# Kernel optimization log

Hardware: AMD Instinct MI355X
Metric: run time of the kernel (lower is better)

The kernel has to match this reference:

```python
import jax, jax.numpy as jnp
from jax import lax
import numpy as np

MAX_ATOMS = 50
MAX_DEGREE = 4
MAX_RINGS = 16
BATCH = 16384
EDGE_KEEP_PROB = 0.3  # fraction of neighbor slots that are real edges; rest are -1 (masked)


def setup_inputs() -> dict:
    key = jax.random.key(0)
    k1, k2 = jax.random.split(key)
    e = jax.random.randint(k1, (BATCH, MAX_ATOMS, MAX_DEGREE), 0, MAX_ATOMS, dtype=jnp.int32)
    keep = jax.random.uniform(k2, (BATCH, MAX_ATOMS, MAX_DEGREE)) < EDGE_KEEP_PROB
    edge = jnp.where(keep, e, jnp.int32(-1))
    return {"edge": edge}


def reference(edge):
    B, A, D = edge.shape
    N = A + 1  # node 0 is the masked-edge sentinel after +1 shift and zero-row pad
    bidx = jnp.arange(B)
    # masked_edges: shift indices by +1, pad a zero row at atom index 0 -> [B, N, D]
    me = jnp.pad(edge.astype(jnp.int32) + 1, ((0, 0), (1, 0), (0, 0)))

    # per-node state, shape [B, N]
    lnf = jnp.ones((B, N), jnp.int32).at[:, 0].set(0).at[:, 1].set(0)  # leaf_not_found
    nnv = jnp.ones((B, N), jnp.int32).at[:, 0].set(0)                  # node_not_visited
    Tree = jnp.zeros((B, N), jnp.int32)                                 # parent pointers
    num_rings = jnp.zeros((B,), jnp.int32)
    ring_idx = jnp.zeros((B, N, 2), jnp.int32)

    def visit(state, visiting):
        lnf, nnv, Tree, num_rings, ring_idx = state
        for d in range(D):  # small static degree loop (4)
            nxt = me[bidx, visiting, d]                 # [B]
            slnf = lnf[bidx, nxt]                       # specific_leaf_not_found
            slnv = nnv[bidx, nxt]                       # specific_leaf_not_visited
            cyc = (1 - slnf) * slnv * (nxt != 0).astype(jnp.int32)  # cycle_found
            ring_idx = ring_idx.at[bidx, num_rings, 0].add(visiting * cyc)
            ring_idx = ring_idx.at[bidx, num_rings, 1].add(nxt * cyc)
            num_rings = num_rings + cyc
            Tree = Tree.at[bidx, nxt].add(slnf * visiting)
            lnf = lnf.at[bidx, nxt].set(0)
        nnv = nnv.at[bidx, visiting].set(0)
        return (lnf, nnv, Tree, num_rings, ring_idx)

    # atom_idx == 1: visit node 1 (special-cased init above)
    state = visit((lnf, nnv, Tree, num_rings, ring_idx), jnp.ones((B,), jnp.int32))

    def atom_body(_, state):
        lnf, nnv = state[0], state[1]
        visiting = jnp.argmax(nnv * (1 - lnf), axis=-1).astype(jnp.int32)
        return visit(state, visiting)

    state = lax.fori_loop(2, A + 1, atom_body, state)
    lnf, nnv, Tree, num_rings, ring_idx = state

    max_num_rings = jnp.max(num_rings)
    rings = jnp.zeros((B, MAX_RINGS, A), jnp.int32)

    def ring_body(carry):
        i, rings = carry
        air = jnp.zeros((B,), jnp.int32)  # atom_in_ring_idx

        # branch 0: mark ancestor chain of ring endpoint 0
        start = ring_idx[:, i, 0]
        vb0 = jnp.zeros((B, N), jnp.int32).at[bidx, start].set(1)
        def mark0(_, c):
            vb0, start = c
            nxt = Tree[bidx, start]
            return (vb0.at[bidx, nxt].set(1), nxt)
        vb0, _ = lax.fori_loop(0, A, mark0, (vb0, start))

        # branch 1: walk ancestor chain of endpoint 1, emit atoms until chains meet
        start = ring_idx[:, i, 1]
        vb1 = jnp.zeros((B, N), jnp.int32).at[bidx, start].set(1)
        rings = rings.at[bidx, i, air].set(start)
        def b1(_, c):
            rings, vb1, start, air = c
            nxt = Tree[bidx, start]
            same = jnp.any(vb0 * vb1 == 1, axis=-1)
            nsv = (~same).astype(jnp.int32)
            air = air + nsv
            rings = rings.at[bidx, i, air].add(nxt * nsv)
            vb1 = vb1.at[bidx, nxt].set(1)
            return (rings, vb1, nxt, air)
        rings, vb1, _, air = lax.fori_loop(0, A, b1, (rings, vb1, start, air))

        # branch 2: walk endpoint-0 chain again, emit atoms until it meets branch 1
        start = ring_idx[:, i, 0]
        vb0b = jnp.zeros((B, N), jnp.int32).at[bidx, start].set(1)
        air = air + 1
        rings = rings.at[bidx, i, air].set(start)
        def b2(_, c):
            rings, vb0b, start, air = c
            nxt = Tree[bidx, start]
            vb0b = vb0b.at[bidx, nxt].set(1)
            same = jnp.any(vb0b * vb1 == 1, axis=-1)
            nsv = (~same).astype(jnp.int32)
            air = air + nsv
            rings = rings.at[bidx, i, air].add(nxt * nsv)
            return (rings, vb0b, nxt, air)
        rings, _, _, _ = lax.fori_loop(0, A, b2, (rings, vb0b, start, air))
        return (i + 1, rings)

    def ring_cond(carry):
        return carry[0] < max_num_rings

    _, rings = lax.while_loop(ring_cond, ring_body, (jnp.int32(0), rings))
    return (Tree, ring_idx, rings - 1)
```

## Files before the change

kernel.cpp:

```cpp
#include <hip/hip_runtime.h>
#include <stdint.h>

constexpr int BATCH = 16384;
constexpr int A     = 50;
constexpr int NN    = 51;
constexpr int MAXR  = 16;
constexpr int EPW   = 8;
constexpr int WPB   = 4;

__global__ __launch_bounds__(WPB * 64)
void fused_kernel(const int* __restrict__ edge, int* __restrict__ out)
{
    const int lane  = threadIdx.x & 63;
    const int wid   = threadIdx.x >> 6;
    const int gbase = (blockIdx.x * WPB + wid) * EPW;

    __shared__ uint32_t eds[WPB][EPW][NN];
    __shared__ uint8_t  tre[WPB][EPW][52];
    __shared__ uint8_t  rg [WPB][EPW][104];

    {
        const uint4 z = make_uint4(0, 0, 0, 0);
        uint4* t16 = (uint4*)&tre[wid][0][0];
        if (lane < 26) t16[lane] = z;
        uint4* r16 = (uint4*)&rg[wid][0][0];
        if (lane < 52) r16[lane] = z;
    }
    {
        const int4* e4 = (const int4*)edge + (size_t)gbase * A;
        #pragma unroll
        for (int k = 0; k < 7; ++k) {
            const int gi = k * 64 + lane;
            if (gi < EPW * A) {
                const int4 v = e4[gi];
                const int el = gi / A, n = gi - A * el;
                eds[wid][el][n] = (uint32_t)(v.x + 1) | ((uint32_t)(v.y + 1) << 8)
                                | ((uint32_t)(v.z + 1) << 16) | ((uint32_t)(v.w + 1) << 24);
            }
        }
    }

    const int  e  = lane >> 3;
    const int  d8 = lane & 7;
    const int  d  = d8 & 3;
    const bool hi = d8 >= 4;

    uint64_t L = (((uint64_t)1 << NN) - 1) & ~(uint64_t)3;
    uint64_t V = (((uint64_t)1 << NN) - 1) & ~(uint64_t)1;
    uint64_t M = 2;
    int visiting = 1, nr = 0;
    uint32_t w = eds[wid][e][0];

    #pragma unroll 1
    for (int it = 0; it < A; ++it) {
        const int n0 = w & 0xff, n1 = (w >> 8) & 0xff, n2 = (w >> 16) & 0xff, n3 = w >> 24;
        const uint64_t bu = ((uint64_t)1 << n0) | ((uint64_t)1 << n1)
                          | ((uint64_t)1 << n2) | ((uint64_t)1 << n3);
        const int myn = (w >> (8 * d)) & 0xff;
        const uint64_t bm = (uint64_t)1 << myn;
        const uint64_t visbit = (uint64_t)1 << visiting;
        const uint64_t Mn = (M | (V & bu)) & ~visbit;
        const bool dn = (Mn == 0);
        const uint64_t Msafe = dn ? (uint64_t)2 : Mn;
        const int nv = (int)__builtin_ctzll(Msafe);
        const uint32_t wn = eds[wid][e][nv - 1];
        const bool dup = ((d > 0) & (myn == n0)) | ((d > 1) & (myn == n1)) | ((d > 2) & (myn == n2));
        const bool fa  = ((L & bm) == 0) | dup;
        const bool cf  = fa & ((V & bm) != 0) & (myn != 0);
        const bool cb  = cf & !hi;
        const uint64_t Bc = __ballot(cb);
        const uint32_t qb = (uint32_t)(Bc >> (lane & 56)) & 0xfu;
        const int slot = nr + __builtin_popcount(qb & ((1u << d) - 1));
        nr += __builtin_popcount(qb);
        tre[wid][e][(fa | hi) ? 51 : myn] = (uint8_t)visiting;
        *(uint16_t*)&rg[wid][e][(cf & hi & (slot < NN)) ? 2 * slot : 102] =
            (uint16_t)(visiting | (myn << 8));
        L &= ~bu;
        V &= ~visbit;
        M = Mn; visiting = nv;
        w = dn ? 0u : wn;
        if (__ballot(!dn) == 0) break;
    }

    int*  otree = out;
    int2* oridx = (int2*)(out + (size_t)BATCH * NN);

    #pragma unroll 1
    for (int e2 = 0; e2 < EPW; ++e2) {
        const int b = gbase + e2;
        const uint32_t pv = (lane < NN) ? *(const uint16_t*)&rg[wid][e2][2 * lane] : 0;
        const int f = (lane < NN) ? (int)tre[wid][e2][lane] : 0;
        if (lane < NN) {
            otree[(size_t)b * NN + lane] = f;
            oridx[(size_t)b * NN + lane] = make_int2((int)(pv & 0xff), (int)(pv >> 8));
        }
        const int r0 = (int)(pv & 0xff), r1 = (int)(pv >> 8);

        uint64_t Mk = ((uint64_t)1 << lane) | ((uint64_t)1 << f);
        int g = f;
        #pragma unroll
        for (int j = 0; j < 6; ++j) {
            const int lo = __builtin_amdgcn_ds_bpermute(g << 2, (int)(uint32_t)Mk);
            const int hh = __builtin_amdgcn_ds_bpermute(g << 2, (int)(Mk >> 32));
            Mk |= ((uint64_t)(uint32_t)hh << 32) | (uint32_t)lo;
            if (j < 5) g = __builtin_amdgcn_ds_bpermute(g << 2, g);
        }
        const int dep = __builtin_popcountll(Mk) - 1;
        const int Mlo = (int)(uint32_t)Mk, Mhi = (int)(Mk >> 32);

        const int a0 = r0 << 2, a1 = r1 << 2;
        const uint64_t set0 = ((uint64_t)(uint32_t)__builtin_amdgcn_ds_bpermute(a0, Mhi) << 32)
                            |  (uint32_t)__builtin_amdgcn_ds_bpermute(a0, Mlo);
        const uint64_t set1 = ((uint64_t)(uint32_t)__builtin_amdgcn_ds_bpermute(a1, Mhi) << 32)
                            |  (uint32_t)__builtin_amdgcn_ds_bpermute(a1, Mlo);
        const int dm  = __builtin_popcountll(set0 & set1) - 1;
        const int ds0 = __builtin_popcountll(set0) - 1;
        const int ds1 = __builtin_popcountll(set1) - 1;
        const int nact = __popcll(__ballot((lane < MAXR) && (r0 != 0)));

        const int s0lo = (int)(uint32_t)set0, s0hi = (int)(set0 >> 32);
        const int s1lo = (int)(uint32_t)set1, s1hi = (int)(set1 >> 32);
        int* orings = out + (size_t)BATCH * NN * 3 + (size_t)b * (MAXR * A);

        for (int i = 0; i < nact; ++i) {
            const uint64_t set0b = ((uint64_t)(uint32_t)__builtin_amdgcn_readlane(s0hi, i) << 32)
                                 |  (uint32_t)__builtin_amdgcn_readlane(s0lo, i);
            const uint64_t set1b = ((uint64_t)(uint32_t)__builtin_amdgcn_readlane(s1hi, i) << 32)
                                 |  (uint32_t)__builtin_amdgcn_readlane(s1lo, i);
            const int dmb  = __builtin_amdgcn_readlane(dm,  i);
            const int ds0b = __builtin_amdgcn_readlane(ds0, i);
            const int ds1b = __builtin_amdgcn_readlane(ds1, i);
            const int s0b  = __builtin_amdgcn_readlane(r0,  i);
            const int tb = ds1b - dmb, tub = tb + ds0b - dmb;

            const bool on1 = ((set1b >> lane) & 1) && (dep >= dmb);
            const bool on0 = ((set0b >> lane) & 1) && (dep >  dmb);
            int pos = on1 ? (ds1b - dep) : on0 ? (tb + 1 + ds0b - dep) : 63;
            pos = pos < 63 ? pos : 63;
            const int pm = __builtin_amdgcn_ds_permute(pos << 2, lane);
            const int rowval = (lane == tb + 1) ? s0b : (lane <= tub ? pm : 0);
            if (lane < A) orings[i * A + lane] = rowval - 1;
        }
        {
            const int startw = nact * A;
            int2* p2 = (int2*)(orings + startw);
            const int n2 = (MAXR * A - startw) >> 1;
            for (int k = lane; k < n2; k += 64) p2[k] = make_int2(-1, -1);
        }
    }
}

extern "C" void kernel_launch(void* const* d_in, const int* in_sizes, int n_in,
                              void* d_out, int out_size, void* d_ws, size_t ws_size,
                              hipStream_t stream) {
    const int* edge = (const int*)d_in[0];
    int* out = (int*)d_out;
    hipLaunchKernelGGL(fused_kernel, dim3(BATCH / (EPW * WPB)), dim3(WPB * 64), 0, stream,
                       edge, out);
}
```

Before: 29.73 us.

## Halve elements per wave, use 16 lanes per molecule, batch ancestor-mask doubling

Each wave now handles 4 molecules instead of 8, with 16 lanes per molecule in the DFS phase. Only 8 of those lanes store results, so the duplicate lanes are masked off. The pointer-doubling ancestor-mask computation is hoisted out of the per-molecule loop and interleaved across the 4 molecules, so independent bpermute chains can overlap. A min-blocks hint of 4 is added to launch_bounds. The aim is to shorten the serial per-wave work and expose more latency hiding, at the cost of twice as many waves and more registers for the unrolled per-molecule arrays.

After: 32.84 us. 1.1x slower.

```diff
diff --git a/kernel.cpp b/kernel.cpp
--- a/kernel.cpp
+++ b/kernel.cpp
@@ -5,10 +5,10 @@
 constexpr int A     = 50;
 constexpr int NN    = 51;
 constexpr int MAXR  = 16;
-constexpr int EPW   = 8;
+constexpr int EPW   = 4;
 constexpr int WPB   = 4;
 
-__global__ __launch_bounds__(WPB * 64)
+__global__ __launch_bounds__(WPB * 64, 4)
 void fused_kernel(const int* __restrict__ edge, int* __restrict__ out)
 {
     const int lane  = threadIdx.x & 63;
@@ -22,14 +22,14 @@
     {
         const uint4 z = make_uint4(0, 0, 0, 0);
         uint4* t16 = (uint4*)&tre[wid][0][0];
-        if (lane < 26) t16[lane] = z;
+        if (lane < 13) t16[lane] = z;
         uint4* r16 = (uint4*)&rg[wid][0][0];
-        if (lane < 52) r16[lane] = z;
+        if (lane < 26) r16[lane] = z;
     }
     {
         const int4* e4 = (const int4*)edge + (size_t)gbase * A;
         #pragma unroll
-        for (int k = 0; k < 7; ++k) {
+        for (int k = 0; k < 4; ++k) {
             const int gi = k * 64 + lane;
             if (gi < EPW * A) {
                 const int4 v = e4[gi];
@@ -40,10 +40,11 @@
         }
     }
 
-    const int  e  = lane >> 3;
-    const int  d8 = lane & 7;
-    const int  d  = d8 & 3;
-    const bool hi = d8 >= 4;
+    const int  e    = lane >> 4;
+    const int  d16  = lane & 15;
+    const int  d    = d16 & 3;
+    const bool hi   = (d16 >> 2) == 1;
+    const bool st8  = d16 < 8;
 
     uint64_t L = (((uint64_t)1 << NN) - 1) & ~(uint64_t)3;
     uint64_t V = (((uint64_t)1 << NN) - 1) & ~(uint64_t)1;
@@ -67,14 +68,16 @@
         const bool dup = ((d > 0) & (myn == n0)) | ((d > 1) & (myn == n1)) | ((d > 2) & (myn == n2));
         const bool fa  = ((L & bm) == 0) | dup;
         const bool cf  = fa & ((V & bm) != 0) & (myn != 0);
-        const bool cb  = cf & !hi;
+        const bool cb  = cf & (d16 < 4);
         const uint64_t Bc = __ballot(cb);
-        const uint32_t qb = (uint32_t)(Bc >> (lane & 56)) & 0xfu;
+        const uint32_t qb = (uint32_t)(Bc >> (lane & 48)) & 0xfu;
         const int slot = nr + __builtin_popcount(qb & ((1u << d) - 1));
         nr += __builtin_popcount(qb);
-        tre[wid][e][(fa | hi) ? 51 : myn] = (uint8_t)visiting;
-        *(uint16_t*)&rg[wid][e][(cf & hi & (slot < NN)) ? 2 * slot : 102] =
-            (uint16_t)(visiting | (myn << 8));
+        if (st8) {
+            tre[wid][e][(fa | hi) ? 51 : myn] = (uint8_t)visiting;
+            *(uint16_t*)&rg[wid][e][(cf & hi & (slot < NN)) ? 2 * slot : 102] =
+                (uint16_t)(visiting | (myn << 8));
+        }
         L &= ~bu;
         V &= ~visbit;
         M = Mn; visiting = nv;
@@ -85,28 +88,41 @@
     int*  otree = out;
     int2* oridx = (int2*)(out + (size_t)BATCH * NN);
 
+    uint64_t MkE[EPW];
+    int gE[EPW];
+    #pragma unroll
+    for (int e2 = 0; e2 < EPW; ++e2) {
+        const int b = gbase + e2;
+        const int f = (lane < NN) ? (int)tre[wid][e2][lane] : 0;
+        MkE[e2] = ((uint64_t)1 << lane) | ((uint64_t)1 << f);
+        gE[e2]  = f;
+        if (lane < NN) {
+            const uint32_t pv = *(const uint16_t*)&rg[wid][e2][2 * lane];
+            otree[(size_t)b * NN + lane] = f;
+            oridx[(size_t)b * NN + lane] = make_int2((int)(pv & 0xff), (int)(pv >> 8));
+        }
+    }
+    #pragma unroll
+    for (int j = 0; j < 6; ++j) {
+        #pragma unroll
+        for (int e2 = 0; e2 < EPW; ++e2) {
+            const int ad = gE[e2] << 2;
+            const int lo = __builtin_amdgcn_ds_bpermute(ad, (int)(uint32_t)MkE[e2]);
+            const int hh = __builtin_amdgcn_ds_bpermute(ad, (int)(MkE[e2] >> 32));
+            MkE[e2] |= ((uint64_t)(uint32_t)hh << 32) | (uint32_t)lo;
+            if (j < 5) gE[e2] = __builtin_amdgcn_ds_bpermute(ad, gE[e2]);
+        }
+    }
+
     #pragma unroll 1
     for (int e2 = 0; e2 < EPW; ++e2) {
         const int b = gbase + e2;
-        const uint32_t pv = (lane < NN) ? *(const uint16_t*)&rg[wid][e2][2 * lane] : 0;
-        const int f = (lane < NN) ? (int)tre[wid][e2][lane] : 0;
-        if (lane < NN) {
-            otree[(size_t)b * NN + lane] = f;
-            oridx[(size_t)b * NN + lane] = make_int2((int)(pv & 0xff), (int)(pv >> 8));
-        }
-        const int r0 = (int)(pv & 0xff), r1 = (int)(pv >> 8);
-
-        uint64_t Mk = ((uint64_t)1 << lane) | ((uint64_t)1 << f);
-        int g = f;
-        #pragma unroll
-        for (int j = 0; j < 6; ++j) {
-            const int lo = __builtin_amdgcn_ds_bpermute(g << 2, (int)(uint32_t)Mk);
-            const int hh = __builtin_amdgcn_ds_bpermute(g << 2, (int)(Mk >> 32));
-            Mk |= ((uint64_t)(uint32_t)hh << 32) | (uint32_t)lo;
-            if (j < 5) g = __builtin_amdgcn_ds_bpermute(g << 2, g);
-        }
+        const uint64_t Mk = MkE[e2];
         const int dep = __builtin_popcountll(Mk) - 1;
         const int Mlo = (int)(uint32_t)Mk, Mhi = (int)(Mk >> 32);
+
+        const uint32_t pv = (lane < NN) ? *(const uint16_t*)&rg[wid][e2][2 * lane] : 0;
+        const int r0 = (int)(pv & 0xff), r1 = (int)(pv >> 8);
 
         const int a0 = r0 << 2, a1 = r1 << 2;
         const uint64_t set0 = ((uint64_t)(uint32_t)__builtin_amdgcn_ds_bpermute(a0, Mhi) << 32)
```

## Interleave pointer-jumping across molecules and unroll ring emission by two

Applied to the files above, without the earlier changes.

Restructures the output phase so the six pointer-jumping bpermute rounds run across all eight molecules of a wave together instead of one molecule at a time. This exposes independent LDS permute operations and hides their latency. The per-ring emission loop is also unrolled by two, packing dm/ds0/ds1 into one register to cut readlane count. The cost is higher VGPR pressure from keeping per-molecule arrays live, which could lower occupancy.

After: 28.77 us. -3.2%, faster.

```diff
diff --git a/kernel.cpp b/kernel.cpp
--- a/kernel.cpp
+++ b/kernel.cpp
@@ -85,29 +85,40 @@
     int*  otree = out;
     int2* oridx = (int2*)(out + (size_t)BATCH * NN);
 
-    #pragma unroll 1
+    uint64_t MkE[EPW];
+    int gE[EPW], r01E[EPW];
+    #pragma unroll
     for (int e2 = 0; e2 < EPW; ++e2) {
         const int b = gbase + e2;
+        const int f = (lane < NN) ? (int)tre[wid][e2][lane] : 0;
         const uint32_t pv = (lane < NN) ? *(const uint16_t*)&rg[wid][e2][2 * lane] : 0;
-        const int f = (lane < NN) ? (int)tre[wid][e2][lane] : 0;
+        MkE[e2] = ((uint64_t)1 << lane) | ((uint64_t)1 << f);
+        gE[e2]  = f;
+        r01E[e2] = (int)pv;
         if (lane < NN) {
             otree[(size_t)b * NN + lane] = f;
             oridx[(size_t)b * NN + lane] = make_int2((int)(pv & 0xff), (int)(pv >> 8));
         }
-        const int r0 = (int)(pv & 0xff), r1 = (int)(pv >> 8);
-
-        uint64_t Mk = ((uint64_t)1 << lane) | ((uint64_t)1 << f);
-        int g = f;
+    }
+    #pragma unroll
+    for (int j = 0; j < 6; ++j) {
         #pragma unroll
-        for (int j = 0; j < 6; ++j) {
-            const int lo = __builtin_amdgcn_ds_bpermute(g << 2, (int)(uint32_t)Mk);
-            const int hh = __builtin_amdgcn_ds_bpermute(g << 2, (int)(Mk >> 32));
-            Mk |= ((uint64_t)(uint32_t)hh << 32) | (uint32_t)lo;
-            if (j < 5) g = __builtin_amdgcn_ds_bpermute(g << 2, g);
-        }
-        const int dep = __builtin_popcountll(Mk) - 1;
+        for (int e2 = 0; e2 < EPW; ++e2) {
+            const int ad = gE[e2] << 2;
+            const int lo = __builtin_amdgcn_ds_bpermute(ad, (int)(uint32_t)MkE[e2]);
+            const int hh = __builtin_amdgcn_ds_bpermute(ad, (int)(MkE[e2] >> 32));
+            MkE[e2] |= ((uint64_t)(uint32_t)hh << 32) | (uint32_t)lo;
+            if (j < 5) gE[e2] = __builtin_amdgcn_ds_bpermute(ad, gE[e2]);
+        }
+    }
+    int depE[EPW], nactE[EPW], packE[EPW];
+    int s0loE[EPW], s0hiE[EPW], s1loE[EPW], s1hiE[EPW];
+    #pragma unroll
+    for (int e2 = 0; e2 < EPW; ++e2) {
+        const uint64_t Mk = MkE[e2];
+        depE[e2] = __builtin_popcountll(Mk) - 1;
         const int Mlo = (int)(uint32_t)Mk, Mhi = (int)(Mk >> 32);
-
+        const int r0 = r01E[e2] & 0xff, r1 = (r01E[e2] >> 8) & 0xff;
         const int a0 = r0 << 2, a1 = r1 << 2;
         const uint64_t set0 = ((uint64_t)(uint32_t)__builtin_amdgcn_ds_bpermute(a0, Mhi) << 32)
                             |  (uint32_t)__builtin_amdgcn_ds_bpermute(a0, Mlo);
@@ -116,37 +127,75 @@
         const int dm  = __builtin_popcountll(set0 & set1) - 1;
         const int ds0 = __builtin_popcountll(set0) - 1;
         const int ds1 = __builtin_popcountll(set1) - 1;
-        const int nact = __popcll(__ballot((lane < MAXR) && (r0 != 0)));
-
-        const int s0lo = (int)(uint32_t)set0, s0hi = (int)(set0 >> 32);
-        const int s1lo = (int)(uint32_t)set1, s1hi = (int)(set1 >> 32);
+        s0loE[e2] = (int)(uint32_t)set0;  s0hiE[e2] = (int)(set0 >> 32);
+        s1loE[e2] = (int)(uint32_t)set1;  s1hiE[e2] = (int)(set1 >> 32);
+        packE[e2] = dm | (ds0 << 8) | (ds1 << 16);
+        nactE[e2] = __popcll(__ballot((lane < MAXR) && (r0 != 0)));
+    }
+
+    #pragma unroll
+    for (int e2 = 0; e2 < EPW; ++e2) {
+        const int b = gbase + e2;
         int* orings = out + (size_t)BATCH * NN * 3 + (size_t)b * (MAXR * A);
-
-        for (int i = 0; i < nact; ++i) {
-            const uint64_t set0b = ((uint64_t)(uint32_t)__builtin_amdgcn_readlane(s0hi, i) << 32)
-                                 |  (uint32_t)__builtin_amdgcn_readlane(s0lo, i);
-            const uint64_t set1b = ((uint64_t)(uint32_t)__builtin_amdgcn_readlane(s1hi, i) << 32)
-                                 |  (uint32_t)__builtin_amdgcn_readlane(s1lo, i);
-            const int dmb  = __builtin_amdgcn_readlane(dm,  i);
-            const int ds0b = __builtin_amdgcn_readlane(ds0, i);
-            const int ds1b = __builtin_amdgcn_readlane(ds1, i);
-            const int s0b  = __builtin_amdgcn_readlane(r0,  i);
+        const int nact = nactE[e2];
+        const int dep  = depE[e2];
+
+        int i = 0;
+        for (; i + 1 < nact; i += 2) {
+            const uint64_t s0a = ((uint64_t)(uint32_t)__builtin_amdgcn_readlane(s0hiE[e2], i) << 32)
+                               |  (uint32_t)__builtin_amdgcn_readlane(s0loE[e2], i);
+            const uint64_t s1a = ((uint64_t)(uint32_t)__builtin_amdgcn_readlane(s1hiE[e2], i) << 32)
+                               |  (uint32_t)__builtin_amdgcn_readlane(s1loE[e2], i);
+            const int pka = __builtin_amdgcn_readlane(packE[e2], i);
+            const int s0va = __builtin_amdgcn_readlane(r01E[e2], i) & 0xff;
+            const int dma = pka & 0xff, ds0a = (pka >> 8) & 0xff, ds1a = (pka >> 16) & 0xff;
+            const int ta = ds1a - dma, tua = ta + ds0a - dma;
+            const bool on1a = ((s1a >> lane) & 1) && (dep >= dma);
+            const bool on0a = ((s0a >> lane) & 1) && (dep >  dma);
+            int posa = on1a ? (ds1a - dep) : on0a ? (ta + 1 + ds0a - dep) : 63;
+            posa = posa < 63 ? posa : 63;
+            const uint64_t s0b = ((uint64_t)(uint32_t)__builtin_amdgcn_readlane(s0hiE[e2], i + 1) << 32)
+                               |  (uint32_t)__builtin_amdgcn_readlane(s0loE[e2], i + 1);
+            const uint64_t s1b = ((uint64_t)(uint32_t)__builtin_amdgcn_readlane(s1hiE[e2], i + 1) << 32)
+                               |  (uint32_t)__builtin_amdgcn_readlane(s1loE[e2], i + 1);
+            const int pkb = __builtin_amdgcn_readlane(packE[e2], i + 1);
+            const int s0vb = __builtin_amdgcn_readlane(r01E[e2], i + 1) & 0xff;
+            const int dmb = pkb & 0xff, ds0b = (pkb >> 8) & 0xff, ds1b = (pkb >> 16) & 0xff;
             const int tb = ds1b - dmb, tub = tb + ds0b - dmb;
-
-            const bool on1 = ((set1b >> lane) & 1) && (dep >= dmb);
-            const bool on0 = ((set0b >> lane) & 1) && (dep >  dmb);
-            int pos = on1 ? (ds1b - dep) : on0 ? (tb + 1 + ds0b - dep) : 63;
-            pos = pos < 63 ? pos : 63;
-            const int pm = __builtin_amdgcn_ds_permute(pos << 2, lane);
-            const int rowval = (lane == tb + 1) ? s0b : (lane <= tub ? pm : 0);
-            if (lane < A) orings[i * A + lane] = rowval - 1;
-        }
-        {
-            const int startw = nact * A;
-            int2* p2 = (int2*)(orings + startw);
-            const int n2 = (MAXR * A - startw) >> 1;
-            for (int k = lane; k < n2; k += 64) p2[k] = make_int2(-1, -1);
-        }
+            const bool on1b = ((s1b >> lane) & 1) && (dep >= dmb);
+            const bool on0b = ((s0b >> lane) & 1) && (dep >  dmb);
+            int posb = on1b ? (ds1b - dep) : on0b ? (tb + 1 + ds0b - dep) : 63;
+            posb = posb < 63 ? posb : 63;
+            const int pma = __builtin_amdgcn_ds_permute(posa << 2, lane);
+            const int pmb = __builtin_amdgcn_ds_permute(posb << 2, lane);
+            const int rva = (lane == ta + 1) ? s0va : (lane <= tua ? pma : 0);
+            const int rvb = (lane == tb + 1) ? s0vb : (lane <= tub ? pmb : 0);
+            if (lane < A) {
+                orings[i * A + lane]       = rva - 1;
+                orings[(i + 1) * A + lane] = rvb - 1;
+            }
+        }
+        if (i < nact) {
+            const uint64_t s0a = ((uint64_t)(uint32_t)__builtin_amdgcn_readlane(s0hiE[e2], i) << 32)
+                               |  (uint32_t)__builtin_amdgcn_readlane(s0loE[e2], i);
+            const uint64_t s1a = ((uint64_t)(uint32_t)__builtin_amdgcn_readlane(s1hiE[e2], i) << 32)
+                               |  (uint32_t)__builtin_amdgcn_readlane(s1loE[e2], i);
+            const int pka = __builtin_amdgcn_readlane(packE[e2], i);
+            const int s0va = __builtin_amdgcn_readlane(r01E[e2], i) & 0xff;
+            const int dma = pka & 0xff, ds0a = (pka >> 8) & 0xff, ds1a = (pka >> 16) & 0xff;
+            const int ta = ds1a - dma, tua = ta + ds0a - dma;
+            const bool on1a = ((s1a >> lane) & 1) && (dep >= dma);
+            const bool on0a = ((s0a >> lane) & 1) && (dep >  dma);
+            int posa = on1a ? (ds1a - dep) : on0a ? (ta + 1 + ds0a - dep) : 63;
+            posa = posa < 63 ? posa : 63;
+            const int pma = __builtin_amdgcn_ds_permute(posa << 2, lane);
+            const int rva = (lane == ta + 1) ? s0va : (lane <= tua ? pma : 0);
+            if (lane < A) orings[i * A + lane] = rva - 1;
+        }
+        const int startw = nact * A;
+        int2* p2 = (int2*)(orings + startw);
+        const int n2 = (MAXR * A - startw) >> 1;
+        for (int k = lane; k < n2; k += 64) p2[k] = make_int2(-1, -1);
     }
 }
 
```
